# Performance work log

Measured on AMD Instinct MI355X. Metric: run time of the kernel, lower is better.

## Reference

```python
import jax, jax.numpy as jnp
import numpy as np

# CycleFC1w1a constants (from init_kwargs / gen_offset)
IN_CH = 384
KH, KW = 1, 7  # cycle kernel; actual conv weight is 1x1
START = (KH * KW) // 2  # 3


def _gen_offset_x(C):
    # kernel_size[0] == 1 branch: off_y = 0, off_x[i] = (i + START) % KW - KW // 2
    i = jnp.arange(C)
    return (i + START) % KW - KW // 2  # int32, values in [-3, 3]


def setup_inputs() -> dict:
    key = jax.random.key(0)
    k1, k2, k3 = jax.random.split(key, 3)
    x = jax.random.normal(k1, (64, IN_CH, 32, 32), dtype=jnp.float32)
    weight = jax.random.normal(k2, (IN_CH, IN_CH), dtype=jnp.float32) * 0.05  # [out_ch, in_ch]
    bias = jax.random.normal(k3, (IN_CH,), dtype=jnp.float32) * 0.01
    return {"x": x, "weight": weight, "bias": bias}


def reference(x, weight, bias):
    B, C, H, W = x.shape
    # BinaryQuantizer forward: sign()
    xb = jnp.sign(x)
    wb = jnp.sign(weight)  # [O, C]

    # Fixed per-channel integer horizontal offsets -> exact shifted gather
    off_x = _gen_offset_x(C)                                  # [C]
    cols = jnp.arange(W)[None, :] + off_x[:, None]            # [C, W] sample col = w + off
    valid = (cols >= 0) & (cols < W)                          # zero-pad out of bounds
    cols_c = jnp.clip(cols, 0, W - 1)
    # gather along width per channel: [B, C, H, W]
    g = jnp.take_along_axis(xb, cols_c[None, :, None, :], axis=3)
    g = g * valid[None, :, None, :].astype(x.dtype)

    # pointwise (1x1) channel-mixing conv
    out = jnp.einsum('bchw,oc->bohw', g, wb) + bias[None, :, None, None]
    return out
```

## Files before the change

kernel.cpp:

```cpp
#include <hip/hip_runtime.h>
#include <stdint.h>


#define IN_CH 384
#define HH 32
#define WW 32
#define BB 64
#define HR 4

constexpr uint64_t P7(int t) {
  uint64_t m = 0;
  for (int k = 0; k < 64; ++k)
    if (k % 7 == t) m |= (1ull << k);
  return m;
}
__device__ __constant__ uint64_t Pm[7] = {P7(0), P7(1), P7(2), P7(3), P7(4), P7(5), P7(6)};

__global__ __launch_bounds__(64) void cyc_prep(const float* __restrict__ wgt,
                                               const float* __restrict__ bias,
                                               uint64_t* __restrict__ wbg,
                                               float* __restrict__ bias2t) {
  const int o = blockIdx.x;
  const int lane = threadIdx.x;
  __shared__ uint64_t wb_sh[6];
#pragma unroll
  for (int j = 0; j < 6; ++j) {
    uint64_t m = __ballot(wgt[o * IN_CH + j * 64 + lane] < 0.0f);
    if (lane == 0) wb_sh[j] = m;
  }
  __syncthreads();
  if (lane < 6) wbg[o * 6 + lane] = wb_sh[lane];
  if (lane < WW) {
    const int w = lane;
    int nv = 0, corr = 0;
#pragma unroll
    for (int j = 0; j < 6; ++j) {
      uint64_t V = 0;
#pragma unroll
      for (int d = -3; d <= 3; ++d) {
        int wd = w + d;
        if (wd >= 0 && wd < WW) V |= Pm[(d - j + 14) % 7];
      }
      nv += __popcll(V);
      corr += __popcll(wb_sh[j] & ~V);
    }
    bias2t[w * IN_CH + o] = bias[o] + (float)nv + 2.0f * (float)corr;
  }
}

__global__ __launch_bounds__(768) void cyc_main(const float* __restrict__ x,
                                                const uint64_t* __restrict__ wbg,
                                                const float* __restrict__ bias2t,
                                                float* __restrict__ out) {
  __shared__ uint64_t sh_X[HR][WW][6];
  __shared__ uint64_t sh_G[HR][WW][6];
  const int t = threadIdx.x;
  const int b = blockIdx.x >> 3;
  const int h0 = (blockIdx.x & 7) * HR;
  const int wave = t >> 6, lane = t & 63;

#pragma unroll
  for (int p = 0; p < 2; ++p) {
    const int tau = wave + p * 12;
    const int r = tau / 6, j = tau % 6;
    const int c = j * 64 + lane;
    const float4* xp = reinterpret_cast<const float4*>(
        x + (size_t)((b * IN_CH + c) * HH + h0 + r) * WW);
    unsigned myw = 0;
#pragma unroll
    for (int i = 0; i < 8; ++i) {
      float4 v = xp[i];
      myw |= (v.x < 0.0f ? 1u : 0u) << (i * 4 + 0);
      myw |= (v.y < 0.0f ? 1u : 0u) << (i * 4 + 1);
      myw |= (v.z < 0.0f ? 1u : 0u) << (i * 4 + 2);
      myw |= (v.w < 0.0f ? 1u : 0u) << (i * 4 + 3);
    }
#pragma unroll
    for (int w = 0; w < WW; ++w) {
      uint64_t m = __ballot((myw >> w) & 1u);
      if (lane == 0) sh_X[r][w][j] = m;
    }
  }
  __syncthreads();

  {
    const int r = t / (WW * 6);
    const int q = t % (WW * 6);
    const int w = q & 31, j = q >> 5;
    uint64_t g = 0;
#pragma unroll
    for (int d = -3; d <= 3; ++d) {
      int wd = w + d;
      if (wd >= 0 && wd < WW) g |= sh_X[r][wd][j] & Pm[(d - j + 14) % 7];
    }
    sh_G[r][w][j] = g;
  }
  __syncthreads();

  const int og = __builtin_amdgcn_readfirstlane(wave);
  const int w = lane & 31, r2 = lane >> 5;
  uint64_t gA[6], gB[6];
  {
    const ulonglong2* gv = reinterpret_cast<const ulonglong2*>(&sh_G[r2][w][0]);
    ulonglong2 a0 = gv[0], a1 = gv[1], a2 = gv[2];
    gA[0] = a0.x; gA[1] = a0.y; gA[2] = a1.x; gA[3] = a1.y; gA[4] = a2.x; gA[5] = a2.y;
    const ulonglong2* hv = reinterpret_cast<const ulonglong2*>(&sh_G[2 + r2][w][0]);
    ulonglong2 b0 = hv[0], b1 = hv[1], b2 = hv[2];
    gB[0] = b0.x; gB[1] = b0.y; gB[2] = b1.x; gB[3] = b1.y; gB[4] = b2.x; gB[5] = b2.y;
  }
  float bb[32];
  {
    const float4* bsrc =
        reinterpret_cast<const float4*>(bias2t + w * IN_CH + og * 32);
    float4* bdst = reinterpret_cast<float4*>(bb);
#pragma unroll
    for (int i = 0; i < 8; ++i) bdst[i] = bsrc[i];
  }
  float* opA = out + ((size_t)b * IN_CH + og * 32) * (HH * WW) + h0 * WW + lane;
  float* opB = opA + 2 * WW;
  const uint64_t* wp = wbg + og * 32 * 6;
#pragma unroll
  for (int i = 0; i < 32; ++i) {
    const uint64_t w0 = wp[i * 6 + 0], w1 = wp[i * 6 + 1], w2 = wp[i * 6 + 2];
    const uint64_t w3 = wp[i * 6 + 3], w4 = wp[i * 6 + 4], w5 = wp[i * 6 + 5];
    int mmA = __popcll(gA[0] ^ w0) + __popcll(gA[1] ^ w1) + __popcll(gA[2] ^ w2) +
              __popcll(gA[3] ^ w3) + __popcll(gA[4] ^ w4) + __popcll(gA[5] ^ w5);
    int mmB = __popcll(gB[0] ^ w0) + __popcll(gB[1] ^ w1) + __popcll(gB[2] ^ w2) +
              __popcll(gB[3] ^ w3) + __popcll(gB[4] ^ w4) + __popcll(gB[5] ^ w5);
    opA[i * (HH * WW)] = bb[i] - 2.0f * (float)mmA;
    opB[i * (HH * WW)] = bb[i] - 2.0f * (float)mmB;
  }
}

extern "C" void kernel_launch(void* const* d_in, const int* in_sizes, int n_in,
                              void* d_out, int out_size, void* d_ws, size_t ws_size,
                              hipStream_t stream) {
  const float* x = (const float*)d_in[0];
  const float* wgt = (const float*)d_in[1];
  const float* bias = (const float*)d_in[2];
  float* out = (float*)d_out;

  uint64_t* wbg = (uint64_t*)d_ws;
  float* bias2t = (float*)((char*)d_ws + IN_CH * 6 * sizeof(uint64_t));

  cyc_prep<<<IN_CH, 64, 0, stream>>>(wgt, bias, wbg, bias2t);
  cyc_main<<<BB * (HH / HR), 768, 0, stream>>>(x, wbg, bias2t, out);
}
```

Measured before the change: 195.6 us.

## Split fused binary conv into separate pack and XOR-popcount GEMM kernels

Breaks the single fused kernel into a pack kernel, which binarizes and shifts x into bitmasks written to a workspace buffer G, and a separate GEMM kernel. The GEMM kernel has 2048 blocks of 256 threads, and each wave computes 48 output channels for 64 pixels. The aim is finer-grained parallelism and better occupancy than the 768-thread fused blocks. The cost is an extra kernel launch plus a global-memory round trip for the packed G buffer (about 3 MB). The fused path remains as a fallback when the workspace is too small.

```diff
diff --git a/kernel.cpp b/kernel.cpp
--- a/kernel.cpp
+++ b/kernel.cpp
@@ -45,6 +45,81 @@
       corr += __popcll(wb_sh[j] & ~V);
     }
     bias2t[w * IN_CH + o] = bias[o] + (float)nv + 2.0f * (float)corr;
+  }
+}
+
+__global__ __launch_bounds__(768) void cyc_pack(const float* __restrict__ x,
+                                                uint64_t* __restrict__ G) {
+  __shared__ uint64_t sh_X[HR][WW][6];
+  const int t = threadIdx.x;
+  const int b = blockIdx.x >> 3;
+  const int h0 = (blockIdx.x & 7) * HR;
+  const int wave = t >> 6, lane = t & 63;
+
+#pragma unroll
+  for (int p = 0; p < 2; ++p) {
+    const int tau = wave + p * 12;
+    const int r = tau / 6, j = tau % 6;
+    const int c = j * 64 + lane;
+    const float4* xp = reinterpret_cast<const float4*>(
+        x + (size_t)((b * IN_CH + c) * HH + h0 + r) * WW);
+    unsigned myw = 0;
+#pragma unroll
+    for (int i = 0; i < 8; ++i) {
+      float4 v = xp[i];
+      myw |= (v.x < 0.0f ? 1u : 0u) << (i * 4 + 0);
+      myw |= (v.y < 0.0f ? 1u : 0u) << (i * 4 + 1);
+      myw |= (v.z < 0.0f ? 1u : 0u) << (i * 4 + 2);
+      myw |= (v.w < 0.0f ? 1u : 0u) << (i * 4 + 3);
+    }
+#pragma unroll
+    for (int w = 0; w < WW; ++w) {
+      uint64_t m = __ballot((myw >> w) & 1u);
+      if (lane == 0) sh_X[r][w][j] = m;
+    }
+  }
+  __syncthreads();
+
+  const int r = t / 192, q = t % 192, w = q / 6, j = q % 6;
+  uint64_t g = 0;
+#pragma unroll
+  for (int d = -3; d <= 3; ++d) {
+    int wd = w + d;
+    if (wd >= 0 && wd < WW) g |= sh_X[r][wd][j] & Pm[(d - j + 14) % 7];
+  }
+  G[(size_t)blockIdx.x * 768 + t] = g;
+}
+
+__global__ __launch_bounds__(256) void cyc_gemm(const uint64_t* __restrict__ G,
+                                                const uint64_t* __restrict__ wbg,
+                                                const float* __restrict__ bias2t,
+                                                float* __restrict__ out) {
+  const int t = threadIdx.x;
+  const int wv = t >> 6, lane = t & 63;
+  const int pg = blockIdx.x >> 1;
+  const int oq = __builtin_amdgcn_readfirstlane(((blockIdx.x & 1) * 4 + wv) * 48);
+  const int b = pg >> 4;
+  const int hw0 = (pg & 15) * 64;
+  const ulonglong2* gp =
+      reinterpret_cast<const ulonglong2*>(G + ((size_t)pg * 64 + lane) * 6);
+  const ulonglong2 q0 = gp[0], q1 = gp[1], q2 = gp[2];
+  const uint64_t g0 = q0.x, g1 = q0.y, g2 = q1.x, g3 = q1.y, g4 = q2.x, g5 = q2.y;
+  const int w = lane & 31;
+  float* op = out + ((size_t)b * IN_CH + oq) * (HH * WW) + hw0 + lane;
+  const uint64_t* wp = wbg + oq * 6;
+  const float* bp = bias2t + w * IN_CH + oq;
+#pragma unroll 1
+  for (int ch = 0; ch < 12; ++ch) {
+    const float4 bb = *reinterpret_cast<const float4*>(bp + ch * 4);
+    const uint64_t* wo = wp + ch * 24;
+#pragma unroll
+    for (int oo = 0; oo < 4; ++oo) {
+      int mm = __popcll(g0 ^ wo[oo * 6 + 0]) + __popcll(g1 ^ wo[oo * 6 + 1]) +
+               __popcll(g2 ^ wo[oo * 6 + 2]) + __popcll(g3 ^ wo[oo * 6 + 3]) +
+               __popcll(g4 ^ wo[oo * 6 + 4]) + __popcll(g5 ^ wo[oo * 6 + 5]);
+      const float bv = (oo == 0) ? bb.x : (oo == 1) ? bb.y : (oo == 2) ? bb.z : bb.w;
+      op[(size_t)(ch * 4 + oo) * (HH * WW)] = bv - 2.0f * (float)mm;
+    }
   }
 }
 
@@ -58,7 +133,6 @@
   const int b = blockIdx.x >> 3;
   const int h0 = (blockIdx.x & 7) * HR;
   const int wave = t >> 6, lane = t & 63;
-
 #pragma unroll
   for (int p = 0; p < 2; ++p) {
     const int tau = wave + p * 12;
@@ -82,7 +156,6 @@
     }
   }
   __syncthreads();
-
   {
     const int r = t / (WW * 6);
     const int q = t % (WW * 6);
@@ -96,7 +169,6 @@
     sh_G[r][w][j] = g;
   }
   __syncthreads();
-
   const int og = __builtin_amdgcn_readfirstlane(wave);
   const int w = lane & 31, r2 = lane >> 5;
   uint64_t gA[6], gB[6];
@@ -108,13 +180,12 @@
     ulonglong2 b0 = hv[0], b1 = hv[1], b2 = hv[2];
     gB[0] = b0.x; gB[1] = b0.y; gB[2] = b1.x; gB[3] = b1.y; gB[4] = b2.x; gB[5] = b2.y;
   }
-  float bb[32];
+  float bbv[32];
   {
-    const float4* bsrc =
-        reinterpret_cast<const float4*>(bias2t + w * IN_CH + og * 32);
-    float4* bdst = reinterpret_cast<float4*>(bb);
-#pragma unroll
-    for (int i = 0; i < 8; ++i) bdst[i] = bsrc[i];
+    const float4* bsrc = reinterpret_cast<const float4*>(bias2t + w * IN_CH);
+    float4* bdst = reinterpret_cast<float4*>(bbv);
+#pragma unroll
+    for (int i = 0; i < 8; ++i) bdst[i] = bsrc[(og * 32) / 4 + i];
   }
   float* opA = out + ((size_t)b * IN_CH + og * 32) * (HH * WW) + h0 * WW + lane;
   float* opB = opA + 2 * WW;
@@ -127,8 +198,8 @@
               __popcll(gA[3] ^ w3) + __popcll(gA[4] ^ w4) + __popcll(gA[5] ^ w5);
     int mmB = __popcll(gB[0] ^ w0) + __popcll(gB[1] ^ w1) + __popcll(gB[2] ^ w2) +
               __popcll(gB[3] ^ w3) + __popcll(gB[4] ^ w4) + __popcll(gB[5] ^ w5);
-    opA[i * (HH * WW)] = bb[i] - 2.0f * (float)mmA;
-    opB[i * (HH * WW)] = bb[i] - 2.0f * (float)mmB;
+    opA[i * (HH * WW)] = bbv[i] - 2.0f * (float)mmA;
+    opB[i * (HH * WW)] = bbv[i] - 2.0f * (float)mmB;
   }
 }
 
@@ -141,8 +212,15 @@
   float* out = (float*)d_out;
 
   uint64_t* wbg = (uint64_t*)d_ws;
-  float* bias2t = (float*)((char*)d_ws + IN_CH * 6 * sizeof(uint64_t));
+  float* bias2t = (float*)((char*)d_ws + 18432);
+  uint64_t* G = (uint64_t*)((char*)d_ws + 18432 + 49152);
+  const size_t need = 18432 + 49152 + (size_t)BB * HH * WW * 6 * 8;
 
   cyc_prep<<<IN_CH, 64, 0, stream>>>(wgt, bias, wbg, bias2t);
-  cyc_main<<<BB * (HH / HR), 768, 0, stream>>>(x, wbg, bias2t, out);
-}
+  if (ws_size >= need) {
+    cyc_pack<<<BB * (HH / HR), 768, 0, stream>>>(x, G);
+    cyc_gemm<<<2048, 256, 0, stream>>>(G, wbg, bias2t, out);
+  } else {
+    cyc_main<<<BB * (HH / HR), 768, 0, stream>>>(x, wbg, bias2t, out);
+  }
+}
```

Measured after the change: 197.2 us. No clear change (+0.8%).
